# Optimization experiments

Hardware: AMD Instinct MI355X
Metric: run time of the kernel (lower is better)

## Reference

```python
import jax, jax.numpy as jnp
import numpy as np

B, H, L, DK, DV = 2, 16, 2048, 64, 64


def setup_inputs() -> dict:
    key = jax.random.key(0)
    kq, kk, kv, km = jax.random.split(key, 4)
    return {
        "Q": jax.random.normal(kq, (B, H, L, DK), dtype=jnp.float32),
        "K": jax.random.normal(kk, (B, H, L, DK), dtype=jnp.float32),
        "V": jax.random.normal(kv, (B, H, L, DV), dtype=jnp.float32),
        "attn_mask": jax.random.uniform(km, (L, L), dtype=jnp.float32),
        "d_k": DK,
    }


def reference(Q, K, V, attn_mask, d_k):
    # scores: [B, H, L, L]
    scale = 1.0 / np.sqrt(d_k).astype(np.float32)
    scores = jnp.einsum("bhqd,bhkd->bhqk", Q, K) * scale
    attn = jax.nn.softmax(scores, axis=-1)
    # MSE-style loss vs a 2-D target mask broadcast over (B, H)
    diff = attn - attn_mask[None, None, :, :]
    loss = jnp.sum(diff * diff)
    context = jnp.einsum("bhqk,bhkd->bhqd", attn, V)
    return (context, loss)
```

## Files before the change

kernel.cpp:

```cpp
#include <hip/hip_runtime.h>

#define NHEAD 32
#define LSEQ  2048
#define DIM   64
#define QBLK  64
#define KBLK  64
#define NTILE (LSEQ / KBLK)

typedef float  f32x4  __attribute__((ext_vector_type(4)));
typedef __bf16 bf16x8 __attribute__((ext_vector_type(8)));
typedef unsigned short u16;

__device__ __forceinline__ u16 f2bf(float f) {
    return __builtin_bit_cast(u16, (__bf16)f);
}
__device__ __forceinline__ void st4bf(u16* p, float4 v) {
    union { u16 h[4]; uint2 q; } pk;
    pk.h[0] = f2bf(v.x); pk.h[1] = f2bf(v.y);
    pk.h[2] = f2bf(v.z); pk.h[3] = f2bf(v.w);
    *(uint2*)p = pk.q;
}
__device__ __forceinline__ bf16x8 comb64(const u16* a, const u16* b) {
    union { uint2 q[2]; bf16x8 v; } u;
    u.q[0] = *(const uint2*)a;
    u.q[1] = *(const uint2*)b;
    return u.v;
}

__device__ __forceinline__ void gl_lds16(const u16* g, u16* l) {
    __builtin_amdgcn_global_load_lds(
        (const __attribute__((address_space(1))) void*)g,
        (__attribute__((address_space(3))) void*)l, 16, 0, 0);
}

#define TILE_SYNC() asm volatile("s_waitcnt vmcnt(0)\n\ts_barrier" ::: "memory")

#define QSCALE 0.18033688011112042f
#define RESCALE_THR 8.0f

__global__ void prepack_kernel(const float* __restrict__ K,
                               const float* __restrict__ V,
                               const float* __restrict__ Msk,
                               u16* __restrict__ wsK, u16* __restrict__ wsV,
                               float* __restrict__ loss)
{
    __shared__ float sv[64][65];
    __shared__ float red2[4];
    const int b = blockIdx.x;
    const int head = b >> 5, kb = b & 31;
    const int t = threadIdx.x;
    const size_t hoff = (size_t)head * LSEQ * DIM;
    const float* Kg = K + hoff + (size_t)(kb * KBLK) * DIM;
    const float* Vg = V + hoff + (size_t)(kb * KBLK) * DIM;
    u16* outK = wsK + (size_t)b * 4096;
    u16* outV = wsV + (size_t)b * 4096;

#pragma unroll
    for (int i = 0; i < 16; ++i) {
        const int e = t + 256 * i;
        sv[e >> 6][e & 63] = Vg[e];
    }
#pragma unroll
    for (int i = 0; i < 2; ++i) {
        const int c = t + 256 * i;
        const int r = c >> 3, q = c & 7;
        const int d0 = 8 * (q ^ (r & 7));
        float4 a  = *(const float4*)(Kg + r * DIM + d0);
        float4 bb = *(const float4*)(Kg + r * DIM + d0 + 4);
        union { u16 h[8]; uint4 u; } pk;
        pk.h[0]=f2bf(a.x);  pk.h[1]=f2bf(a.y);  pk.h[2]=f2bf(a.z);  pk.h[3]=f2bf(a.w);
        pk.h[4]=f2bf(bb.x); pk.h[5]=f2bf(bb.y); pk.h[6]=f2bf(bb.z); pk.h[7]=f2bf(bb.w);
        *(uint4*)(outK + c * 8) = pk.u;
    }
    __syncthreads();
#pragma unroll
    for (int i = 0; i < 2; ++i) {
        const int c = t + 256 * i;
        const int d = c >> 3, q = c & 7;
        const int cl = q ^ (d & 7);
        const int mp = cl >> 2, lq = cl & 3;
        union { u16 h[8]; uint4 u; } pk;
#pragma unroll
        for (int s = 0; s < 2; ++s) {
            const int k0 = 4 * (8 * mp + 4 * s + lq);
#pragma unroll
            for (int j = 0; j < 4; ++j)
                pk.h[4 * s + j] = f2bf(sv[k0 + j][d]);
        }
        *(uint4*)(outV + c * 8) = pk.u;
    }

    float s = 0.f;
    const float4* mq = (const float4*)(Msk + (size_t)b * 4096);
#pragma unroll
    for (int i = 0; i < 4; ++i) {
        float4 v = mq[t + 256 * i];
        s += v.x * v.x + v.y * v.y + v.z * v.z + v.w * v.w;
    }
#pragma unroll
    for (int off = 1; off <= 32; off <<= 1) s += __shfl_xor(s, off);
    if ((t & 63) == 0) red2[t >> 6] = s;
    __syncthreads();
    if (t == 0)
        atomicAdd(loss, 32.0f * (red2[0] + red2[1] + red2[2] + red2[3]));
}

#define LDMASK(kb, M)                                                          \
    {                                                                          \
        const float* mp_ = Msk + (size_t)qg * LSEQ + (kb) * KBLK + 4 * lq;     \
        M##0 = *(const f32x4*)(mp_);                                           \
        M##1 = *(const f32x4*)(mp_ + 16);                                      \
        M##2 = *(const f32x4*)(mp_ + 32);                                      \
        M##3 = *(const f32x4*)(mp_ + 48);                                      \
    }

#define SMPART(Sm, Mm, base)                                                   \
    {                                                                          \
        _Pragma("unroll")                                                      \
        for (int r = 0; r < 4; ++r) {                                          \
            float p = __builtin_amdgcn_exp2f(Sm[r] - mrun);                    \
            psum += p;                                                         \
            pp2  += p * p;                                                     \
            ppm  += p * Mm[r];                                                 \
            pb[(base) + r] = f2bf(p);                                          \
        }                                                                      \
    }

#define BODY(BUF, M)                                                           \
    {                                                                          \
        f32x4 S[4];                                                            \
        __builtin_amdgcn_s_setprio(1);                                         \
        _Pragma("unroll")                                                      \
        for (int m = 0; m < 4; ++m) {                                          \
            const u16* kro = &lds_k[BUF][(16 * m + lr) * 64];                  \
            bf16x8 kf0 = *(const bf16x8*)(kro + ((lq ^ x7) << 3));             \
            bf16x8 kf1 = *(const bf16x8*)(kro + (((lq + 4) ^ x7) << 3));       \
            f32x4 z = (f32x4){0.f, 0.f, 0.f, 0.f};                             \
            z = __builtin_amdgcn_mfma_f32_16x16x32_bf16(kf0, qf[0], z, 0, 0, 0); \
            z = __builtin_amdgcn_mfma_f32_16x16x32_bf16(kf1, qf[1], z, 0, 0, 0); \
            S[m] = z;                                                          \
        }                                                                      \
        __builtin_amdgcn_s_setprio(0);                                         \
         \
        float tm = fmaxf(fmaxf(fmaxf(S[0][0], S[0][1]), fmaxf(S[0][2], S[0][3])), \
                         fmaxf(fmaxf(S[1][0], S[1][1]), fmaxf(S[1][2], S[1][3]))); \
        tm = fmaxf(tm, fmaxf(fmaxf(fmaxf(S[2][0], S[2][1]), fmaxf(S[2][2], S[2][3])), \
                             fmaxf(fmaxf(S[3][0], S[3][1]), fmaxf(S[3][2], S[3][3])))); \
        if (!__all(tm - mrun <= RESCALE_THR)) {                                \
            tm = fmaxf(tm, __shfl_xor(tm, 16));                                \
            tm = fmaxf(tm, __shfl_xor(tm, 32));                                \
            const float mn = fmaxf(mrun, tm);                                  \
            const float al = __builtin_amdgcn_exp2f(mrun - mn);                \
            mrun = mn;                                                         \
            lrun *= al; la2 *= al * al; lam *= al;                             \
            _Pragma("unroll")                                                  \
            for (int dt = 0; dt < 4; ++dt) acc[dt] *= al;                      \
        }                                                                      \
        float psum = 0.f, pp2 = 0.f, ppm = 0.f;                                \
        u16 pb[16];                                                            \
        SMPART(S[0], M##0, 0)                                                  \
        SMPART(S[1], M##1, 4)                                                  \
        SMPART(S[2], M##2, 8)                                                  \
        SMPART(S[3], M##3, 12)                                                 \
        lrun += psum; la2 += pp2; lam += ppm;                                  \
        bf16x8 pf[2];                                                          \
        _Pragma("unroll")                                                      \
        for (int mp = 0; mp < 2; ++mp) {                                       \
            union { u16 h[8]; bf16x8 v; } u;                                   \
            _Pragma("unroll")                                                  \
            for (int j = 0; j < 4; ++j) {                                      \
                u.h[j] = pb[8 * mp + j]; u.h[4 + j] = pb[8 * mp + 4 + j];      \
            }                                                                  \
            pf[mp] = u.v;                                                      \
        }                                                                      \
        __builtin_amdgcn_s_setprio(1);                                         \
        _Pragma("unroll")                                                      \
        for (int dt = 0; dt < 4; ++dt) {                                       \
            const u16* vro = &lds_v[BUF][(16 * dt + lr) * 64];                 \
            _Pragma("unroll")                                                  \
            for (int mp = 0; mp < 2; ++mp) {                                   \
                bf16x8 vf = *(const bf16x8*)(vro + (((4 * mp + lq) ^ x7) << 3)); \
                acc[dt] = __builtin_amdgcn_mfma_f32_16x16x32_bf16(vf, pf[mp],  \
                                                                  acc[dt], 0, 0, 0); \
            }                                                                  \
        }                                                                      \
        __builtin_amdgcn_s_setprio(0);                                         \
    }

__launch_bounds__(256, 4)
__global__ void attn_fused_kernel(const float* __restrict__ Q,
                                  const u16* __restrict__ wsK,
                                  const u16* __restrict__ wsV,
                                  const float* __restrict__ Msk,
                                  float* __restrict__ out,
                                  float* __restrict__ loss)
{
    __shared__ __align__(16) u16 lds_k[2][4096];
    __shared__ __align__(16) u16 lds_v[2][4096];

    const int t  = threadIdx.x;
    const int wg   = ((int)blockIdx.x & 7) * 128 + ((int)blockIdx.x >> 3);
    const int head = wg >> 5;
    const int qb   = wg & 31;
    const int qbase = qb * QBLK;
    const int w  = t >> 6;
    const int l  = t & 63;
    const int lr = l & 15;
    const int lq = l >> 4;
    const int x7 = lr & 7;

    const size_t hoff = (size_t)head * LSEQ * DIM;
    const int qg = qbase + 16 * w + lr;

    bf16x8 qf[2];
#pragma unroll
    for (int s = 0; s < 2; ++s) {
        const float* src = Q + hoff + (size_t)qg * DIM + 32 * s + 8 * lq;
        float4 a = *(const float4*)(src);
        float4 b = *(const float4*)(src + 4);
        union { u16 h[8]; bf16x8 v; } u;
        u.h[0] = f2bf(a.x * QSCALE); u.h[1] = f2bf(a.y * QSCALE);
        u.h[2] = f2bf(a.z * QSCALE); u.h[3] = f2bf(a.w * QSCALE);
        u.h[4] = f2bf(b.x * QSCALE); u.h[5] = f2bf(b.y * QSCALE);
        u.h[6] = f2bf(b.z * QSCALE); u.h[7] = f2bf(b.w * QSCALE);
        qf[s] = u.v;
    }

    f32x4 acc[4];
#pragma unroll
    for (int dt = 0; dt < 4; ++dt) acc[dt] = (f32x4){0.f, 0.f, 0.f, 0.f};
    float mrun = -1e30f, lrun = 0.f, la2 = 0.f, lam = 0.f;

    const u16* srcK = wsK + (size_t)(head * NTILE) * 4096 + t * 8;
    const u16* srcV = wsV + (size_t)(head * NTILE) * 4096 + t * 8;

    auto stage = [&](int buf, int kb) {
        const u16* gk = srcK + (size_t)kb * 4096;
        const u16* gv = srcV + (size_t)kb * 4096;
        gl_lds16(gk,        &lds_k[buf][t * 8]);
        gl_lds16(gk + 2048, &lds_k[buf][t * 8 + 2048]);
        gl_lds16(gv,        &lds_v[buf][t * 8]);
        gl_lds16(gv + 2048, &lds_v[buf][t * 8 + 2048]);
    };

    f32x4 mA0, mA1, mA2, mA3, mB0, mB1, mB2, mB3;

    stage(0, 0);
    LDMASK(0, mA);

    for (int kb = 0; kb < NTILE; kb += 2) {
        TILE_SYNC();
        stage(1, kb + 1);
        LDMASK(kb + 1, mB);
        BODY(0, mA);

        TILE_SYNC();
        if (kb + 2 < NTILE) {
            stage(0, kb + 2);
            LDMASK(kb + 2, mA);
        }
        BODY(1, mB);
    }

#pragma unroll
    for (int off = 16; off <= 32; off <<= 1) {
        lrun += __shfl_xor(lrun, off);
        la2  += __shfl_xor(la2,  off);
        lam  += __shfl_xor(lam,  off);
    }

    const float inv = 1.0f / lrun;

#pragma unroll
    for (int dt = 0; dt < 4; ++dt) {
        float4 o;
        o.x = acc[dt][0] * inv; o.y = acc[dt][1] * inv;
        o.z = acc[dt][2] * inv; o.w = acc[dt][3] * inv;
        *(float4*)(out + hoff + (size_t)qg * DIM + 16 * dt + 4 * lq) = o;
    }

    float part = la2 * inv * inv - 2.0f * lam * inv;
    part = (l < 16) ? part : 0.f;
#pragma unroll
    for (int off = 1; off <= 8; off <<= 1) part += __shfl_xor(part, off);
    if (l == 0) atomicAdd(loss, part);
}

__global__ void masksq_kernel(const float* __restrict__ Msk, float* __restrict__ loss)
{
    __shared__ float red[4];
    float s = 0.f;
    const size_t n4 = (size_t)LSEQ * LSEQ / 4;
    for (size_t i = (size_t)blockIdx.x * blockDim.x + threadIdx.x; i < n4;
         i += (size_t)gridDim.x * blockDim.x) {
        float4 v = ((const float4*)Msk)[i];
        s += v.x * v.x + v.y * v.y + v.z * v.z + v.w * v.w;
    }
#pragma unroll
    for (int off = 1; off <= 32; off <<= 1) s += __shfl_xor(s, off);
    if ((threadIdx.x & 63) == 0) red[threadIdx.x >> 6] = s;
    __syncthreads();
    if (threadIdx.x == 0) {
        float tot = red[0] + red[1] + red[2] + red[3];
        atomicAdd(loss, 32.0f * tot);
    }
}

__launch_bounds__(256, 4)
__global__ void attn_fallback_kernel(const float* __restrict__ Q,
                                     const float* __restrict__ K,
                                     const float* __restrict__ V,
                                     const float* __restrict__ Msk,
                                     float* __restrict__ out,
                                     float* __restrict__ loss)
{
    __shared__ __align__(16) u16 lds_k[64][72];
    __shared__ __align__(16) u16 lds_v[64][68];

    const int t  = threadIdx.x;
    const int wg   = ((int)blockIdx.x & 7) * 128 + ((int)blockIdx.x >> 3);
    const int head = wg >> 5;
    const int qb   = wg & 31;
    const int qbase = qb * QBLK;
    const int w  = t >> 6;
    const int l  = t & 63;
    const int lr = l & 15;
    const int lq = l >> 4;

    const size_t hoff = (size_t)head * LSEQ * DIM;
    const int qg = qbase + 16 * w + lr;

    bf16x8 qf[2];
#pragma unroll
    for (int s = 0; s < 2; ++s) {
        const float* src = Q + hoff + (size_t)qg * DIM + 32 * s + 8 * lq;
        float4 a = *(const float4*)(src);
        float4 b = *(const float4*)(src + 4);
        union { u16 h[8]; bf16x8 v; } u;
        u.h[0] = f2bf(a.x * QSCALE); u.h[1] = f2bf(a.y * QSCALE);
        u.h[2] = f2bf(a.z * QSCALE); u.h[3] = f2bf(a.w * QSCALE);
        u.h[4] = f2bf(b.x * QSCALE); u.h[5] = f2bf(b.y * QSCALE);
        u.h[6] = f2bf(b.z * QSCALE); u.h[7] = f2bf(b.w * QSCALE);
        qf[s] = u.v;
    }

    f32x4 acc[4];
#pragma unroll
    for (int dt = 0; dt < 4; ++dt) acc[dt] = (f32x4){0.f, 0.f, 0.f, 0.f};
    float mrun = -1e30f, lrun = 0.f, la2 = 0.f, lam = 0.f;

    for (int kb = 0; kb < NTILE; ++kb) {
        const int kbase = kb * KBLK;
        __syncthreads();
        f32x4 mreg[4];
        {
            const float* mp_ = Msk + (size_t)qg * LSEQ + kbase + 4 * lq;
#pragma unroll
            for (int m = 0; m < 4; ++m)
                mreg[m] = *(const f32x4*)(mp_ + 16 * m);
        }
        {
            const float* Kg = K + hoff + (size_t)kbase * DIM;
            const float* Vg = V + hoff + (size_t)kbase * DIM;
#pragma unroll
            for (int i = 0; i < 4; ++i) {
                const int id = t + 256 * i;
                const int r = id >> 4, c = (id & 15) * 4;
                float4 kv = *(const float4*)(Kg + r * DIM + c);
                float4 vv = *(const float4*)(Vg + r * DIM + c);
                st4bf(&lds_k[r][c], kv);
                lds_v[c + 0][r] = f2bf(vv.x);
                lds_v[c + 1][r] = f2bf(vv.y);
                lds_v[c + 2][r] = f2bf(vv.z);
                lds_v[c + 3][r] = f2bf(vv.w);
            }
        }
        __syncthreads();

        f32x4 S[4];
#pragma unroll
        for (int m = 0; m < 4; ++m) {
            bf16x8 kf0 = *(const bf16x8*)&lds_k[16 * m + lr][8 * lq];
            bf16x8 kf1 = *(const bf16x8*)&lds_k[16 * m + lr][32 + 8 * lq];
            f32x4 z = (f32x4){0.f, 0.f, 0.f, 0.f};
            z = __builtin_amdgcn_mfma_f32_16x16x32_bf16(kf0, qf[0], z, 0, 0, 0);
            z = __builtin_amdgcn_mfma_f32_16x16x32_bf16(kf1, qf[1], z, 0, 0, 0);
            S[m] = z;
        }

        float tm = fmaxf(fmaxf(fmaxf(S[0][0], S[0][1]), fmaxf(S[0][2], S[0][3])),
                         fmaxf(fmaxf(S[1][0], S[1][1]), fmaxf(S[1][2], S[1][3])));
        tm = fmaxf(tm, fmaxf(fmaxf(fmaxf(S[2][0], S[2][1]), fmaxf(S[2][2], S[2][3])),
                             fmaxf(fmaxf(S[3][0], S[3][1]), fmaxf(S[3][2], S[3][3]))));
        tm = fmaxf(tm, __shfl_xor(tm, 16));
        tm = fmaxf(tm, __shfl_xor(tm, 32));
        if (!__all(tm - mrun <= RESCALE_THR)) {
            const float mn = fmaxf(mrun, tm);
            const float al = __builtin_amdgcn_exp2f(mrun - mn);
            mrun = mn;
            lrun *= al; la2 *= al * al; lam *= al;
#pragma unroll
            for (int dt = 0; dt < 4; ++dt) acc[dt] *= al;
        }

        float psum = 0.f, pp2 = 0.f, ppm = 0.f;
        u16 pb[16];
#pragma unroll
        for (int m = 0; m < 4; ++m) {
#pragma unroll
            for (int r = 0; r < 4; ++r) {
                float p = __builtin_amdgcn_exp2f(S[m][r] - mrun);
                psum += p;
                pp2  += p * p;
                ppm  += p * mreg[m][r];
                pb[4 * m + r] = f2bf(p);
            }
        }
        lrun += psum; la2 += pp2; lam += ppm;

        bf16x8 pf[2];
#pragma unroll
        for (int mp = 0; mp < 2; ++mp) {
            union { u16 h[8]; bf16x8 v; } u;
#pragma unroll
            for (int j = 0; j < 4; ++j) { u.h[j] = pb[8 * mp + j]; u.h[4 + j] = pb[8 * mp + 4 + j]; }
            pf[mp] = u.v;
        }
#pragma unroll
        for (int dt = 0; dt < 4; ++dt) {
#pragma unroll
            for (int mp = 0; mp < 2; ++mp) {
                bf16x8 vf = comb64(&lds_v[16 * dt + lr][32 * mp + 4 * lq],
                                   &lds_v[16 * dt + lr][32 * mp + 16 + 4 * lq]);
                acc[dt] = __builtin_amdgcn_mfma_f32_16x16x32_bf16(vf, pf[mp], acc[dt], 0, 0, 0);
            }
        }
    }

#pragma unroll
    for (int off = 16; off <= 32; off <<= 1) {
        lrun += __shfl_xor(lrun, off);
        la2  += __shfl_xor(la2,  off);
        lam  += __shfl_xor(lam,  off);
    }
    const float inv = 1.0f / lrun;
#pragma unroll
    for (int dt = 0; dt < 4; ++dt) {
        float4 o;
        o.x = acc[dt][0] * inv; o.y = acc[dt][1] * inv;
        o.z = acc[dt][2] * inv; o.w = acc[dt][3] * inv;
        *(float4*)(out + hoff + (size_t)qg * DIM + 16 * dt + 4 * lq) = o;
    }
    float part = la2 * inv * inv - 2.0f * lam * inv;
    part = (l < 16) ? part : 0.f;
#pragma unroll
    for (int off = 1; off <= 8; off <<= 1) part += __shfl_xor(part, off);
    if (l == 0) atomicAdd(loss, part);
}

extern "C" void kernel_launch(void* const* d_in, const int* in_sizes, int n_in,
                              void* d_out, int out_size, void* d_ws, size_t ws_size,
                              hipStream_t stream)
{
    const float* Q   = (const float*)d_in[0];
    const float* K   = (const float*)d_in[1];
    const float* V   = (const float*)d_in[2];
    const float* Msk = (const float*)d_in[3];
    float* out  = (float*)d_out;
    float* loss = out + (size_t)NHEAD * LSEQ * DIM;

    hipMemsetAsync(loss, 0, sizeof(float), stream);

    const size_t need = (size_t)2 * NHEAD * NTILE * 4096 * sizeof(u16);
    if (d_ws && ws_size >= need) {
        u16* wsK = (u16*)d_ws;
        u16* wsV = wsK + (size_t)NHEAD * NTILE * 4096;
        prepack_kernel<<<NHEAD * NTILE, 256, 0, stream>>>(K, V, Msk, wsK, wsV, loss);
        attn_fused_kernel<<<NHEAD * (LSEQ / QBLK), 256, 0, stream>>>(Q, wsK, wsV, Msk, out, loss);
    } else {
        masksq_kernel<<<256, 256, 0, stream>>>(Msk, loss);
        attn_fallback_kernel<<<NHEAD * (LSEQ / QBLK), 256, 0, stream>>>(Q, K, V, Msk, out, loss);
    }
}
```

Baseline: 150.8 us.

## Software-pipeline QK of next tile with softmax and PV of current tile

Restructures the attention main loop so that the QK^T MFMAs for tile k+1 are issued before the softmax and PV work for tile k. V moves to a triple-buffered LDS ring while K stays double-buffered, and the mask loads shift to match. The aim is to overlap matrix-core work with the exp/reduction VALU work and hide LDS latency. In exchange it holds an extra set of score registers and 8 KB more LDS per block, which may reduce occupancy or cause spills.

After: 145.9 us, median of 2. -3.2%, faster.

```diff
diff --git a/kernel.cpp b/kernel.cpp
--- a/kernel.cpp
+++ b/kernel.cpp
@@ -105,47 +105,62 @@
         atomicAdd(loss, 32.0f * (red2[0] + red2[1] + red2[2] + red2[3]));
 }
 
-#define LDMASK(kb, M)                                                          \
-    {                                                                          \
-        const float* mp_ = Msk + (size_t)qg * LSEQ + (kb) * KBLK + 4 * lq;     \
-        M##0 = *(const f32x4*)(mp_);                                           \
-        M##1 = *(const f32x4*)(mp_ + 16);                                      \
-        M##2 = *(const f32x4*)(mp_ + 32);                                      \
-        M##3 = *(const f32x4*)(mp_ + 48);                                      \
+#define STAGE(tile, kbuf, vbuf)                                                \
+    {                                                                          \
+        const u16* gk = srcK + (size_t)(tile) * 4096;                          \
+        const u16* gv = srcV + (size_t)(tile) * 4096;                          \
+        gl_lds16(gk,        &lds_k[kbuf][t * 8]);                              \
+        gl_lds16(gk + 2048, &lds_k[kbuf][t * 8 + 2048]);                       \
+        gl_lds16(gv,        &lds_v[vbuf][t * 8]);                              \
+        gl_lds16(gv + 2048, &lds_v[vbuf][t * 8 + 2048]);                       \
+    }
+
+#define LDMASK(kb_)                                                            \
+    {                                                                          \
+        const float* mp_ = Msk + (size_t)qg * LSEQ + (kb_) * KBLK + 4 * lq;    \
+        mM0 = *(const f32x4*)(mp_);                                            \
+        mM1 = *(const f32x4*)(mp_ + 16);                                       \
+        mM2 = *(const f32x4*)(mp_ + 32);                                       \
+        mM3 = *(const f32x4*)(mp_ + 48);                                       \
+    }
+
+#define QK1(kb_, mm, Sdst)                                                     \
+    {                                                                          \
+        const u16* kro = (kb_) + (16 * (mm) + lr) * 64;                        \
+        bf16x8 kf0 = *(const bf16x8*)(kro + ((lq ^ x7) << 3));                 \
+        bf16x8 kf1 = *(const bf16x8*)(kro + (((lq + 4) ^ x7) << 3));           \
+        f32x4 z = (f32x4){0.f, 0.f, 0.f, 0.f};                                 \
+        z = __builtin_amdgcn_mfma_f32_16x16x32_bf16(kf0, qf[0], z, 0, 0, 0);   \
+        z = __builtin_amdgcn_mfma_f32_16x16x32_bf16(kf1, qf[1], z, 0, 0, 0);   \
+        Sdst = z;                                                              \
+    }
+
+#define QK(kbuf, SD0, SD1, SD2, SD3)                                           \
+    {                                                                          \
+        const u16* kb_ = &lds_k[kbuf][0];                                      \
+        __builtin_amdgcn_s_setprio(1);                                         \
+        QK1(kb_, 0, SD0) QK1(kb_, 1, SD1) QK1(kb_, 2, SD2) QK1(kb_, 3, SD3)    \
+        __builtin_amdgcn_s_setprio(0);                                         \
     }
 
 #define SMPART(Sm, Mm, base)                                                   \
     {                                                                          \
         _Pragma("unroll")                                                      \
         for (int r = 0; r < 4; ++r) {                                          \
-            float p = __builtin_amdgcn_exp2f(Sm[r] - mrun);                    \
-            psum += p;                                                         \
-            pp2  += p * p;                                                     \
-            ppm  += p * Mm[r];                                                 \
-            pb[(base) + r] = f2bf(p);                                          \
+            float pe = __builtin_amdgcn_exp2f(Sm[r] - mrun);                   \
+            psum += pe;                                                        \
+            pp2  += pe * pe;                                                   \
+            ppm  += pe * Mm[r];                                                \
+            pb[(base) + r] = f2bf(pe);                                         \
         }                                                                      \
     }
 
-#define BODY(BUF, M)                                                           \
-    {                                                                          \
-        f32x4 S[4];                                                            \
-        __builtin_amdgcn_s_setprio(1);                                         \
-        _Pragma("unroll")                                                      \
-        for (int m = 0; m < 4; ++m) {                                          \
-            const u16* kro = &lds_k[BUF][(16 * m + lr) * 64];                  \
-            bf16x8 kf0 = *(const bf16x8*)(kro + ((lq ^ x7) << 3));             \
-            bf16x8 kf1 = *(const bf16x8*)(kro + (((lq + 4) ^ x7) << 3));       \
-            f32x4 z = (f32x4){0.f, 0.f, 0.f, 0.f};                             \
-            z = __builtin_amdgcn_mfma_f32_16x16x32_bf16(kf0, qf[0], z, 0, 0, 0); \
-            z = __builtin_amdgcn_mfma_f32_16x16x32_bf16(kf1, qf[1], z, 0, 0, 0); \
-            S[m] = z;                                                          \
-        }                                                                      \
-        __builtin_amdgcn_s_setprio(0);                                         \
-         \
-        float tm = fmaxf(fmaxf(fmaxf(S[0][0], S[0][1]), fmaxf(S[0][2], S[0][3])), \
-                         fmaxf(fmaxf(S[1][0], S[1][1]), fmaxf(S[1][2], S[1][3]))); \
-        tm = fmaxf(tm, fmaxf(fmaxf(fmaxf(S[2][0], S[2][1]), fmaxf(S[2][2], S[2][3])), \
-                             fmaxf(fmaxf(S[3][0], S[3][1]), fmaxf(S[3][2], S[3][3])))); \
+#define SMF(SS0, SS1, SS2, SS3)                                                \
+    {                                                                          \
+        float tm = fmaxf(fmaxf(fmaxf(SS0[0], SS0[1]), fmaxf(SS0[2], SS0[3])),  \
+                         fmaxf(fmaxf(SS1[0], SS1[1]), fmaxf(SS1[2], SS1[3]))); \
+        tm = fmaxf(tm, fmaxf(fmaxf(fmaxf(SS2[0], SS2[1]), fmaxf(SS2[2], SS2[3])), \
+                             fmaxf(fmaxf(SS3[0], SS3[1]), fmaxf(SS3[2], SS3[3])))); \
         if (!__all(tm - mrun <= RESCALE_THR)) {                                \
             tm = fmaxf(tm, __shfl_xor(tm, 16));                                \
             tm = fmaxf(tm, __shfl_xor(tm, 32));                                \
@@ -158,34 +173,39 @@
         }                                                                      \
         float psum = 0.f, pp2 = 0.f, ppm = 0.f;                                \
         u16 pb[16];                                                            \
-        SMPART(S[0], M##0, 0)                                                  \
-        SMPART(S[1], M##1, 4)                                                  \
-        SMPART(S[2], M##2, 8)                                                  \
-        SMPART(S[3], M##3, 12)                                                 \
+        SMPART(SS0, mM0, 0) SMPART(SS1, mM1, 4)                                \
+        SMPART(SS2, mM2, 8) SMPART(SS3, mM3, 12)                               \
         lrun += psum; la2 += pp2; lam += ppm;                                  \
-        bf16x8 pf[2];                                                          \
-        _Pragma("unroll")                                                      \
-        for (int mp = 0; mp < 2; ++mp) {                                       \
+        {                                                                      \
             union { u16 h[8]; bf16x8 v; } u;                                   \
-            _Pragma("unroll")                                                  \
-            for (int j = 0; j < 4; ++j) {                                      \
-                u.h[j] = pb[8 * mp + j]; u.h[4 + j] = pb[8 * mp + 4 + j];      \
-            }                                                                  \
-            pf[mp] = u.v;                                                      \
+            u.h[0] = pb[0]; u.h[1] = pb[1]; u.h[2] = pb[2]; u.h[3] = pb[3];    \
+            u.h[4] = pb[4]; u.h[5] = pb[5]; u.h[6] = pb[6]; u.h[7] = pb[7];    \
+            pf0 = u.v;                                                         \
         }                                                                      \
+        {                                                                      \
+            union { u16 h[8]; bf16x8 v; } u;                                   \
+            u.h[0] = pb[8];  u.h[1] = pb[9];  u.h[2] = pb[10]; u.h[3] = pb[11];\
+            u.h[4] = pb[12]; u.h[5] = pb[13]; u.h[6] = pb[14]; u.h[7] = pb[15];\
+            pf1 = u.v;                                                         \
+        }                                                                      \
+    }
+
+#define PV(vidx)                                                               \
+    {                                                                          \
+        const u16* vb_ = &lds_v[vidx][0];                                      \
         __builtin_amdgcn_s_setprio(1);                                         \
         _Pragma("unroll")                                                      \
         for (int dt = 0; dt < 4; ++dt) {                                       \
-            const u16* vro = &lds_v[BUF][(16 * dt + lr) * 64];                 \
-            _Pragma("unroll")                                                  \
-            for (int mp = 0; mp < 2; ++mp) {                                   \
-                bf16x8 vf = *(const bf16x8*)(vro + (((4 * mp + lq) ^ x7) << 3)); \
-                acc[dt] = __builtin_amdgcn_mfma_f32_16x16x32_bf16(vf, pf[mp],  \
-                                                                  acc[dt], 0, 0, 0); \
-            }                                                                  \
+            const u16* vro = vb_ + (16 * dt + lr) * 64;                        \
+            bf16x8 vfa = *(const bf16x8*)(vro + ((lq ^ x7) << 3));             \
+            bf16x8 vfb = *(const bf16x8*)(vro + (((4 + lq) ^ x7) << 3));       \
+            acc[dt] = __builtin_amdgcn_mfma_f32_16x16x32_bf16(vfa, pf0, acc[dt], 0, 0, 0); \
+            acc[dt] = __builtin_amdgcn_mfma_f32_16x16x32_bf16(vfb, pf1, acc[dt], 0, 0, 0); \
         }                                                                      \
         __builtin_amdgcn_s_setprio(0);                                         \
     }
+
+#define ROT3(x) x = ((x) == 2) ? 0 : ((x) + 1);
 
 __launch_bounds__(256, 4)
 __global__ void attn_fused_kernel(const float* __restrict__ Q,
@@ -196,7 +216,7 @@
                                   float* __restrict__ loss)
 {
     __shared__ __align__(16) u16 lds_k[2][4096];
-    __shared__ __align__(16) u16 lds_v[2][4096];
+    __shared__ __align__(16) u16 lds_v[3][4096];
 
     const int t  = threadIdx.x;
     const int wg   = ((int)blockIdx.x & 7) * 128 + ((int)blockIdx.x >> 3);
@@ -234,33 +254,45 @@
     const u16* srcK = wsK + (size_t)(head * NTILE) * 4096 + t * 8;
     const u16* srcV = wsV + (size_t)(head * NTILE) * 4096 + t * 8;
 
-    auto stage = [&](int buf, int kb) {
-        const u16* gk = srcK + (size_t)kb * 4096;
-        const u16* gv = srcV + (size_t)kb * 4096;
-        gl_lds16(gk,        &lds_k[buf][t * 8]);
-        gl_lds16(gk + 2048, &lds_k[buf][t * 8 + 2048]);
-        gl_lds16(gv,        &lds_v[buf][t * 8]);
-        gl_lds16(gv + 2048, &lds_v[buf][t * 8 + 2048]);
-    };
-
-    f32x4 mA0, mA1, mA2, mA3, mB0, mB1, mB2, mB3;
-
-    stage(0, 0);
-    LDMASK(0, mA);
-
-    for (int kb = 0; kb < NTILE; kb += 2) {
+    f32x4 S_a0, S_a1, S_a2, S_a3, S_b0, S_b1, S_b2, S_b3;
+    f32x4 mM0, mM1, mM2, mM3;
+    bf16x8 pf0, pf1;
+
+    STAGE(0, 0, 0);
+    TILE_SYNC();
+    STAGE(1, 1, 1);
+    QK(0, S_a0, S_a1, S_a2, S_a3);
+    TILE_SYNC();
+
+    int vr = 0, vw = 2;
+
+    for (int kp = 1; kp <= 29; kp += 2) {
+        STAGE(kp + 1, 0, vw);
+        LDMASK(kp - 1);
+        QK(1, S_b0, S_b1, S_b2, S_b3);
+        SMF(S_a0, S_a1, S_a2, S_a3);
+        PV(vr);
         TILE_SYNC();
-        stage(1, kb + 1);
-        LDMASK(kb + 1, mB);
-        BODY(0, mA);
-
+        ROT3(vr); ROT3(vw);
+
+        STAGE(kp + 2, 1, vw);
+        LDMASK(kp);
+        QK(0, S_a0, S_a1, S_a2, S_a3);
+        SMF(S_b0, S_b1, S_b2, S_b3);
+        PV(vr);
         TILE_SYNC();
-        if (kb + 2 < NTILE) {
-            stage(0, kb + 2);
-            LDMASK(kb + 2, mA);
-        }
-        BODY(1, mB);
-    }
+        ROT3(vr); ROT3(vw);
+    }
+
+    LDMASK(30);
+    QK(1, S_b0, S_b1, S_b2, S_b3);
+    SMF(S_a0, S_a1, S_a2, S_a3);
+    PV(vr);
+    ROT3(vr);
+
+    LDMASK(31);
+    SMF(S_b0, S_b1, S_b2, S_b3);
+    PV(vr);
 
 #pragma unroll
     for (int off = 16; off <= 32; off <<= 1) {
```
